# Performance work log

Measured on AMD Instinct MI355X. Metric: run time of the kernel, lower is better.

## Reference

```python
import jax, jax.numpy as jnp
import numpy as np

N_Q = 32   # query window / partition increment
N_K = 128  # key window length
H = 8      # heads


def _ln(x, w=None, b=None, eps=1e-5):
    m = jnp.mean(x, axis=-1, keepdims=True)
    v = jnp.var(x, axis=-1, keepdims=True)
    y = (x - m) * jax.lax.rsqrt(v + eps)
    if w is not None:
        y = y * w
    if b is not None:
        y = y + b
    return y


def setup_inputs() -> dict:
    key = jax.random.key(0)
    ks = jax.random.split(key, 16)
    B, N, C, CP = 1, 2048, 128, 16
    sc = 1.0 / np.sqrt(C)
    inp = {
        "x": jax.random.normal(ks[0], (B, N, C), jnp.float32),
        "s": jax.random.normal(ks[1], (B, N, C), jnp.float32),
        "pair": jax.random.normal(ks[2], (B, N, N, CP), jnp.float32),
        "adaln_s_w": jnp.ones((C,), jnp.float32),
        "adaln_gate_w": jax.random.normal(ks[3], (C, C), jnp.float32) * sc,
        "adaln_gate_b": jnp.zeros((C,), jnp.float32),
        "adaln_skip_w": jax.random.normal(ks[4], (C, C), jnp.float32) * sc,
        "q_w": jax.random.normal(ks[5], (C, C), jnp.float32) * sc,
        "q_b": jnp.zeros((C,), jnp.float32),
        "k_w": jax.random.normal(ks[6], (C, C), jnp.float32) * sc,
        "v_w": jax.random.normal(ks[7], (C, C), jnp.float32) * sc,
        "pair_ln_w": jnp.ones((CP,), jnp.float32),
        "pair_ln_b": jnp.zeros((CP,), jnp.float32),
        "pair_proj_w": jax.random.normal(ks[8], (CP, H), jnp.float32) * 0.25,
        "gate_w": jax.random.normal(ks[9], (C, C), jnp.float32) * sc,
        "attn_proj_w": jax.random.normal(ks[10], (C, C), jnp.float32) * sc,
        "out_w": jax.random.normal(ks[11], (C, C), jnp.float32) * sc,
        "out_b": jnp.full((C,), -2.0, jnp.float32),
    }
    return inp


def reference(x, s, pair, adaln_s_w, adaln_gate_w, adaln_gate_b, adaln_skip_w,
              q_w, q_b, k_w, v_w, pair_ln_w, pair_ln_b, pair_proj_w,
              gate_w, attn_proj_w, out_w, out_b):
    B, N, C = x.shape
    nb = N // N_Q          # number of local blocks
    pad = (N_K - N_Q) // 2  # 48: zero halo on each side
    hd = C // H

    # AdaLN: LN(a) no affine; LN(s) scale-only; gate + skip from s
    a = _ln(x)
    sn = _ln(s, adaln_s_w)
    a = jax.nn.sigmoid(sn @ adaln_gate_w + adaln_gate_b) * a + sn @ adaln_skip_w

    q = a @ q_w + q_b
    k = a @ k_w
    v = a @ v_w

    # local windows: window i covers padded[32i : 32i+128]
    idx = N_Q * jnp.arange(nb)[:, None] + jnp.arange(N_K)[None, :]  # [nb, N_K]

    def window(t):  # [B,N,C] -> [B,nb,N_K,C] with zero-padded edges
        tp = jnp.pad(t, ((0, 0), (pad, pad), (0, 0)))
        return tp[:, idx]

    qb = q.reshape(B, nb, N_Q, H, hd).transpose(0, 3, 1, 2, 4)        # [B,H,nb,NQ,hd]
    kb = window(k).reshape(B, nb, N_K, H, hd).transpose(0, 3, 1, 2, 4)
    vb = window(v).reshape(B, nb, N_K, H, hd).transpose(0, 3, 1, 2, 4)

    # pair bias -> local blocks [B,H,nb,NQ,NK]
    pb = _ln(pair, pair_ln_w, pair_ln_b) @ pair_proj_w                # [B,N,N,H]
    pb = pb.reshape(B, nb, N_Q, N, H)
    pb = jnp.pad(pb, ((0, 0), (0, 0), (0, 0), (pad, pad), (0, 0)))
    pb = jnp.take_along_axis(pb, idx[None, :, None, :, None], axis=3)  # [B,nb,NQ,NK,H]
    bias = pb.transpose(0, 4, 1, 2, 3)

    logits = jnp.einsum('bhnqd,bhnkd->bhnqk', qb, kb) / jnp.sqrt(jnp.float32(hd)) + bias
    attn = jax.nn.softmax(logits, axis=-1)
    o = jnp.einsum('bhnqk,bhnkd->bhnqd', attn, vb)
    o = o.transpose(0, 2, 3, 1, 4).reshape(B, N, C)

    g = jax.nn.sigmoid(o @ gate_w) * o
    out = g @ attn_proj_w
    out = jax.nn.sigmoid(out @ out_w + out_b) * out
    return out
```

## Files before the change

kernel.cpp:

```cpp
#include <hip/hip_runtime.h>
#include <math.h>

#define NTOK 2048
#define CDIM 128
#define HHEADS 8
#define HDIM 16
#define NQW 32
#define NKW 128
#define PADW 48
#define CPD 16
#define BT 8

__device__ __forceinline__ float sigmoid_(float z){ return 1.0f/(1.0f+__expf(-z)); }
__device__ __forceinline__ float rdlane(float v, int l){
    return __int_as_float(__builtin_amdgcn_readlane(__float_as_int(v), l));
}

__global__ __launch_bounds__(512, 4) void k_front(
    const float* __restrict__ x, const float* __restrict__ s,
    const float* __restrict__ s_w,
    const float* __restrict__ gate_w, const float* __restrict__ gate_b,
    const float* __restrict__ skip_w,
    const float* __restrict__ q_w, const float* __restrict__ q_b,
    const float* __restrict__ k_w, const float* __restrict__ v_w,
    const float* __restrict__ pair, const float* __restrict__ pln_w,
    const float* __restrict__ pln_b, const float* __restrict__ pproj,
    float* __restrict__ qo, float* __restrict__ ko, float* __restrict__ vo,
    float* __restrict__ bias)
{
    __shared__ float act_t[CDIM][10];
    __shared__ float sn_t[CDIM][10];
    __shared__ float part[8][2][BT][CDIM];
    const int tid = threadIdx.x;
    const int bid = blockIdx.x;

    if (bid >= NTOK/BT) {
        #pragma unroll
        for (int rep = 0; rep < 2; ++rep) {
            const int idx = (bid - NTOK/BT) * 1024 + rep*512 + tid;
            const int qg = idx >> 7;
            const int j  = idx & 127;
            const int ib = qg >> 5;
            const int qr = qg & 31;
            const int kg = (ib << 5) - PADW + j;
            float outh[HHEADS] = {0,0,0,0,0,0,0,0};
            if (kg >= 0 && kg < NTOK) {
                const float* p = pair + ((size_t)qg * NTOK + kg) * CPD;
                float buf[CPD];
                float sum = 0.f, ssq = 0.f;
                #pragma unroll
                for (int c = 0; c < CPD; c += 4) {
                    const float4 t4 = *(const float4*)(p + c);
                    buf[c+0]=t4.x; buf[c+1]=t4.y; buf[c+2]=t4.z; buf[c+3]=t4.w;
                    sum += t4.x+t4.y+t4.z+t4.w;
                    ssq += t4.x*t4.x+t4.y*t4.y+t4.z*t4.z+t4.w*t4.w;
                }
                const float m  = sum * (1.0f/CPD);
                const float vr = ssq * (1.0f/CPD) - m*m;
                const float rs = rsqrtf(vr + 1e-5f);
                #pragma unroll
                for (int c = 0; c < CPD; ++c) {
                    const float y = (buf[c]-m)*rs*pln_w[c] + pln_b[c];
                    #pragma unroll
                    for (int h = 0; h < HHEADS; ++h)
                        outh[h] = fmaf(y, pproj[c*HHEADS+h], outh[h]);
                }
            }
            float* bb = bias + ((size_t)(ib*HHEADS)*NQW + qr)*NKW + j;
            #pragma unroll
            for (int h = 0; h < HHEADS; ++h)
                bb[(size_t)h*NQW*NKW] = outh[h];
        }
        return;
    }

    const int tok0 = bid * BT;
    const int w = tid >> 6;
    const int L = tid & 63;

    {
        const float2 xv = *(const float2*)(x + (size_t)(tok0+w)*CDIM + 2*L);
        const float2 yv = *(const float2*)(s + (size_t)(tok0+w)*CDIM + 2*L);
        float sx = xv.x+xv.y, sxx = xv.x*xv.x+xv.y*xv.y;
        float sy = yv.x+yv.y, syy = yv.x*yv.x+yv.y*yv.y;
        #pragma unroll
        for (int m = 1; m < 64; m <<= 1) {
            sx  += __shfl_xor(sx,  m, 64);
            sxx += __shfl_xor(sxx, m, 64);
            sy  += __shfl_xor(sy,  m, 64);
            syy += __shfl_xor(syy, m, 64);
        }
        const float inv = 1.0f/128.0f;
        const float mx = sx*inv, vx = sxx*inv - mx*mx;
        const float my = sy*inv, vy = syy*inv - my*my;
        const float rx = rsqrtf(vx+1e-5f), ry = rsqrtf(vy+1e-5f);
        const float2 swv = *(const float2*)(s_w + 2*L);
        act_t[2*L][w]   = (xv.x-mx)*rx;
        act_t[2*L+1][w] = (xv.y-mx)*rx;
        sn_t[2*L][w]    = (yv.x-my)*ry*swv.x;
        sn_t[2*L+1][w]  = (yv.y-my)*ry*swv.y;
    }
    __syncthreads();

    const int i0 = w * 16;
    float snr0 = sn_t[i0 + (L>>3)][L&7];
    float snr1 = sn_t[i0 + 8 + (L>>3)][L&7];

    float ag[8][2] = {{0}}, as_[8][2] = {{0}};
    #pragma unroll
    for (int ii = 0; ii < 16; ++ii) {
        const float2 wg  = *(const float2*)(gate_w + (size_t)(i0+ii)*CDIM + 2*L);
        const float2 wsk = *(const float2*)(skip_w + (size_t)(i0+ii)*CDIM + 2*L);
        #pragma unroll
        for (int t = 0; t < 8; ++t) {
            const int v = ii*8 + t;
            const float a = rdlane((v < 64) ? snr0 : snr1, v & 63);
            ag[t][0]  = fmaf(a, wg.x,  ag[t][0]);
            ag[t][1]  = fmaf(a, wg.y,  ag[t][1]);
            as_[t][0] = fmaf(a, wsk.x, as_[t][0]);
            as_[t][1] = fmaf(a, wsk.y, as_[t][1]);
        }
    }
    #pragma unroll
    for (int t = 0; t < 8; ++t) {
        *(float2*)&part[w][0][t][2*L] = make_float2(ag[t][0],  ag[t][1]);
        *(float2*)&part[w][1][t][2*L] = make_float2(as_[t][0], as_[t][1]);
    }
    __syncthreads();

    const int j  = tid & 127;
    const int tq = tid >> 7;
    {
        float zg[2] = {0,0}, zs[2] = {0,0};
        #pragma unroll
        for (int ww = 0; ww < 8; ++ww) {
            #pragma unroll
            for (int tt = 0; tt < 2; ++tt) {
                zg[tt] += part[ww][0][2*tq+tt][j];
                zs[tt] += part[ww][1][2*tq+tt][j];
            }
        }
        const float gb = gate_b[j];
        const float2 av = *(const float2*)&act_t[j][2*tq];
        const float a2x = sigmoid_(zg[0]+gb)*av.x + zs[0];
        const float a2y = sigmoid_(zg[1]+gb)*av.y + zs[1];
        *(float2*)&sn_t[j][2*tq] = make_float2(a2x, a2y);
    }
    __syncthreads();

    float ar0 = sn_t[i0 + (L>>3)][L&7];
    float ar1 = sn_t[i0 + 8 + (L>>3)][L&7];
    float aq[8][2] = {{0}}, ak[8][2] = {{0}}, avv[8][2] = {{0}};
    #pragma unroll
    for (int ii = 0; ii < 16; ++ii) {
        const float2 wq = *(const float2*)(q_w + (size_t)(i0+ii)*CDIM + 2*L);
        const float2 wk = *(const float2*)(k_w + (size_t)(i0+ii)*CDIM + 2*L);
        const float2 wv = *(const float2*)(v_w + (size_t)(i0+ii)*CDIM + 2*L);
        #pragma unroll
        for (int t = 0; t < 8; ++t) {
            const int v = ii*8 + t;
            const float a = rdlane((v < 64) ? ar0 : ar1, v & 63);
            aq[t][0]  = fmaf(a, wq.x, aq[t][0]);
            aq[t][1]  = fmaf(a, wq.y, aq[t][1]);
            ak[t][0]  = fmaf(a, wk.x, ak[t][0]);
            ak[t][1]  = fmaf(a, wk.y, ak[t][1]);
            avv[t][0] = fmaf(a, wv.x, avv[t][0]);
            avv[t][1] = fmaf(a, wv.y, avv[t][1]);
        }
    }
    #pragma unroll
    for (int t = 0; t < 8; ++t) {
        *(float2*)&part[w][0][t][2*L] = make_float2(aq[t][0], aq[t][1]);
        *(float2*)&part[w][1][t][2*L] = make_float2(ak[t][0], ak[t][1]);
    }
    __syncthreads();
    {
        float zq[2] = {0,0}, zk[2] = {0,0};
        #pragma unroll
        for (int ww = 0; ww < 8; ++ww) {
            #pragma unroll
            for (int tt = 0; tt < 2; ++tt) {
                zq[tt] += part[ww][0][2*tq+tt][j];
                zk[tt] += part[ww][1][2*tq+tt][j];
            }
        }
        const float qbj = q_b[j];
        #pragma unroll
        for (int tt = 0; tt < 2; ++tt) {
            const size_t row = (size_t)(tok0 + 2*tq + tt)*CDIM + j;
            qo[row] = zq[tt] + qbj;
            ko[row] = zk[tt];
        }
    }
    __syncthreads();
    #pragma unroll
    for (int t = 0; t < 8; ++t)
        *(float2*)&part[w][0][t][2*L] = make_float2(avv[t][0], avv[t][1]);
    __syncthreads();
    {
        float zv[2] = {0,0};
        #pragma unroll
        for (int ww = 0; ww < 8; ++ww) {
            #pragma unroll
            for (int tt = 0; tt < 2; ++tt)
                zv[tt] += part[ww][0][2*tq+tt][j];
        }
        #pragma unroll
        for (int tt = 0; tt < 2; ++tt)
            vo[(size_t)(tok0 + 2*tq + tt)*CDIM + j] = zv[tt];
    }
}

__global__ __launch_bounds__(256) void k_attn(
    const float* __restrict__ qi, const float* __restrict__ ki,
    const float* __restrict__ vi, const float* __restrict__ bias,
    float* __restrict__ o)
{
    __shared__ float khs[NKW*20];
    __shared__ float vts[HDIM*132];
    __shared__ float Pms[NQW*132];
    const int ib = blockIdx.x;
    const int h  = blockIdx.y;
    const int t  = threadIdx.x;

    {
        const int jr  = t >> 1;
        const int d08 = (t & 1) * 8;
        const int kg  = ib*NQW - PADW + jr;
        float4 k0 = {0,0,0,0}, k1 = {0,0,0,0};
        float4 v0 = {0,0,0,0}, v1 = {0,0,0,0};
        if (kg >= 0 && kg < NTOK) {
            const float* sk = ki + (size_t)kg*CDIM + h*HDIM + d08;
            const float* sv = vi + (size_t)kg*CDIM + h*HDIM + d08;
            k0 = *(const float4*)sk;  k1 = *(const float4*)(sk+4);
            v0 = *(const float4*)sv;  v1 = *(const float4*)(sv+4);
        }
        *(float4*)&khs[jr*20 + d08]     = k0;
        *(float4*)&khs[jr*20 + d08 + 4] = k1;
        vts[(d08+0)*132 + jr] = v0.x;
        vts[(d08+1)*132 + jr] = v0.y;
        vts[(d08+2)*132 + jr] = v0.z;
        vts[(d08+3)*132 + jr] = v0.w;
        vts[(d08+4)*132 + jr] = v1.x;
        vts[(d08+5)*132 + jr] = v1.y;
        vts[(d08+6)*132 + jr] = v1.z;
        vts[(d08+7)*132 + jr] = v1.w;
    }
    __syncthreads();

    {
        const int rp = t >> 4;
        const int ln = t & 15;
        const int q0 = 2*rp;
        float4 qv[2][4];
        #pragma unroll
        for (int i = 0; i < 2; ++i) {
            const float4* qp = (const float4*)(qi + (size_t)(ib*NQW + q0 + i)*CDIM + h*HDIM);
            #pragma unroll
            for (int dq = 0; dq < 4; ++dq) qv[i][dq] = qp[dq];
        }
        const float* br = bias + ((size_t)(ib*HHEADS + h)*NQW + q0)*NKW;
        float acc[2][8];
        #pragma unroll
        for (int m2 = 0; m2 < 8; ++m2) {
            const int k = ln + 16*m2;
            const float4 c0 = *(const float4*)&khs[k*20];
            const float4 c1 = *(const float4*)&khs[k*20 + 4];
            const float4 c2 = *(const float4*)&khs[k*20 + 8];
            const float4 c3 = *(const float4*)&khs[k*20 + 12];
            #pragma unroll
            for (int i = 0; i < 2; ++i) {
                float sdot = qv[i][0].x*c0.x;
                sdot = fmaf(qv[i][0].y, c0.y, sdot);
                sdot = fmaf(qv[i][0].z, c0.z, sdot);
                sdot = fmaf(qv[i][0].w, c0.w, sdot);
                sdot = fmaf(qv[i][1].x, c1.x, sdot);
                sdot = fmaf(qv[i][1].y, c1.y, sdot);
                sdot = fmaf(qv[i][1].z, c1.z, sdot);
                sdot = fmaf(qv[i][1].w, c1.w, sdot);
                sdot = fmaf(qv[i][2].x, c2.x, sdot);
                sdot = fmaf(qv[i][2].y, c2.y, sdot);
                sdot = fmaf(qv[i][2].z, c2.z, sdot);
                sdot = fmaf(qv[i][2].w, c2.w, sdot);
                sdot = fmaf(qv[i][3].x, c3.x, sdot);
                sdot = fmaf(qv[i][3].y, c3.y, sdot);
                sdot = fmaf(qv[i][3].z, c3.z, sdot);
                sdot = fmaf(qv[i][3].w, c3.w, sdot);
                acc[i][m2] = sdot*0.25f + br[(size_t)i*NKW + k];
            }
        }
        #pragma unroll
        for (int i = 0; i < 2; ++i) {
            float mx = acc[i][0];
            #pragma unroll
            for (int m2 = 1; m2 < 8; ++m2) mx = fmaxf(mx, acc[i][m2]);
            mx = fmaxf(mx, __shfl_xor(mx, 1, 64));
            mx = fmaxf(mx, __shfl_xor(mx, 2, 64));
            mx = fmaxf(mx, __shfl_xor(mx, 4, 64));
            mx = fmaxf(mx, __shfl_xor(mx, 8, 64));
            float sm = 0.f;
            #pragma unroll
            for (int m2 = 0; m2 < 8; ++m2) { acc[i][m2] = __expf(acc[i][m2]-mx); sm += acc[i][m2]; }
            sm += __shfl_xor(sm, 1, 64);
            sm += __shfl_xor(sm, 2, 64);
            sm += __shfl_xor(sm, 4, 64);
            sm += __shfl_xor(sm, 8, 64);
            const float invs = 1.0f / sm;
            #pragma unroll
            for (int m2 = 0; m2 < 8; ++m2)
                Pms[(q0+i)*132 + ln + 16*m2] = acc[i][m2]*invs;
        }
    }
    __syncthreads();

    {
        const int qr = t >> 3, d0 = t & 7;
        const float* pr  = &Pms[qr*132];
        const float* vp0 = &vts[d0*132];
        const float* vp1 = &vts[(d0+8)*132];
        float a0 = 0.f, a1 = 0.f;
        #pragma unroll
        for (int k4 = 0; k4 < 32; ++k4) {
            const float4 pm = *(const float4*)(pr  + 4*k4);
            const float4 u0 = *(const float4*)(vp0 + 4*k4);
            const float4 u1 = *(const float4*)(vp1 + 4*k4);
            a0 = fmaf(pm.x, u0.x, a0); a0 = fmaf(pm.y, u0.y, a0);
            a0 = fmaf(pm.z, u0.z, a0); a0 = fmaf(pm.w, u0.w, a0);
            a1 = fmaf(pm.x, u1.x, a1); a1 = fmaf(pm.y, u1.y, a1);
            a1 = fmaf(pm.z, u1.z, a1); a1 = fmaf(pm.w, u1.w, a1);
        }
        float* dst = o + (size_t)(ib*NQW + qr)*CDIM + h*HDIM;
        dst[d0]   = a0;
        dst[d0+8] = a1;
    }
}

__global__ __launch_bounds__(512) void k_back(
    const float* __restrict__ oin, const float* __restrict__ gate_w,
    const float* __restrict__ proj_w, const float* __restrict__ out_w,
    const float* __restrict__ out_b, float* __restrict__ out)
{
    __shared__ float b0_t[CDIM][10];
    __shared__ float b1_t[CDIM][10];
    __shared__ float part[8][BT][CDIM];
    const int tid = threadIdx.x;
    const int tok0 = blockIdx.x * BT;
    const int w = tid >> 6, L = tid & 63;
    const int j = tid & 127, tq = tid >> 7;

    {
        const float2 ov = *(const float2*)(oin + (size_t)tok0*CDIM + 2*tid);
        const int e = 2*tid, c = e & 127, t = e >> 7;
        b0_t[c][t]   = ov.x;
        b0_t[c+1][t] = ov.y;
    }
    __syncthreads();

    const int i0 = w * 16;

    {
        const float r0 = b0_t[i0 + (L>>3)][L&7];
        const float r1 = b0_t[i0 + 8 + (L>>3)][L&7];
        float acc[8][2] = {{0}};
        #pragma unroll
        for (int ii = 0; ii < 16; ++ii) {
            const float2 wv = *(const float2*)(gate_w + (size_t)(i0+ii)*CDIM + 2*L);
            #pragma unroll
            for (int t = 0; t < 8; ++t) {
                const int v = ii*8 + t;
                const float a = rdlane((v < 64) ? r0 : r1, v & 63);
                acc[t][0] = fmaf(a, wv.x, acc[t][0]);
                acc[t][1] = fmaf(a, wv.y, acc[t][1]);
            }
        }
        #pragma unroll
        for (int t = 0; t < 8; ++t)
            *(float2*)&part[w][t][2*L] = make_float2(acc[t][0], acc[t][1]);
    }
    __syncthreads();
    {
        float z[2] = {0,0};
        #pragma unroll
        for (int ww = 0; ww < 8; ++ww) {
            z[0] += part[ww][2*tq][j];
            z[1] += part[ww][2*tq+1][j];
        }
        const float2 ov = *(const float2*)&b0_t[j][2*tq];
        *(float2*)&b1_t[j][2*tq] = make_float2(sigmoid_(z[0])*ov.x, sigmoid_(z[1])*ov.y);
    }
    __syncthreads();

    {
        const float r0 = b1_t[i0 + (L>>3)][L&7];
        const float r1 = b1_t[i0 + 8 + (L>>3)][L&7];
        float acc[8][2] = {{0}};
        #pragma unroll
        for (int ii = 0; ii < 16; ++ii) {
            const float2 wv = *(const float2*)(proj_w + (size_t)(i0+ii)*CDIM + 2*L);
            #pragma unroll
            for (int t = 0; t < 8; ++t) {
                const int v = ii*8 + t;
                const float a = rdlane((v < 64) ? r0 : r1, v & 63);
                acc[t][0] = fmaf(a, wv.x, acc[t][0]);
                acc[t][1] = fmaf(a, wv.y, acc[t][1]);
            }
        }
        #pragma unroll
        for (int t = 0; t < 8; ++t)
            *(float2*)&part[w][t][2*L] = make_float2(acc[t][0], acc[t][1]);
    }
    __syncthreads();
    float t2v[2];
    {
        float z[2] = {0,0};
        #pragma unroll
        for (int ww = 0; ww < 8; ++ww) {
            z[0] += part[ww][2*tq][j];
            z[1] += part[ww][2*tq+1][j];
        }
        t2v[0] = z[0]; t2v[1] = z[1];
        *(float2*)&b0_t[j][2*tq] = make_float2(z[0], z[1]);
    }
    __syncthreads();

    {
        const float r0 = b0_t[i0 + (L>>3)][L&7];
        const float r1 = b0_t[i0 + 8 + (L>>3)][L&7];
        float acc[8][2] = {{0}};
        #pragma unroll
        for (int ii = 0; ii < 16; ++ii) {
            const float2 wv = *(const float2*)(out_w + (size_t)(i0+ii)*CDIM + 2*L);
            #pragma unroll
            for (int t = 0; t < 8; ++t) {
                const int v = ii*8 + t;
                const float a = rdlane((v < 64) ? r0 : r1, v & 63);
                acc[t][0] = fmaf(a, wv.x, acc[t][0]);
                acc[t][1] = fmaf(a, wv.y, acc[t][1]);
            }
        }
        #pragma unroll
        for (int t = 0; t < 8; ++t)
            *(float2*)&part[w][t][2*L] = make_float2(acc[t][0], acc[t][1]);
    }
    __syncthreads();
    {
        float z[2] = {0,0};
        #pragma unroll
        for (int ww = 0; ww < 8; ++ww) {
            z[0] += part[ww][2*tq][j];
            z[1] += part[ww][2*tq+1][j];
        }
        const float ob = out_b[j];
        out[(size_t)(tok0 + 2*tq)*CDIM + j]     = sigmoid_(z[0]+ob)*t2v[0];
        out[(size_t)(tok0 + 2*tq + 1)*CDIM + j] = sigmoid_(z[1]+ob)*t2v[1];
    }
}

extern "C" void kernel_launch(void* const* d_in, const int* in_sizes, int n_in,
                              void* d_out, int out_size, void* d_ws, size_t ws_size,
                              hipStream_t stream) {
    (void)in_sizes; (void)n_in; (void)out_size; (void)ws_size;
    const float* x           = (const float*)d_in[0];
    const float* s           = (const float*)d_in[1];
    const float* pair        = (const float*)d_in[2];
    const float* adaln_s_w   = (const float*)d_in[3];
    const float* adaln_gate_w= (const float*)d_in[4];
    const float* adaln_gate_b= (const float*)d_in[5];
    const float* adaln_skip_w= (const float*)d_in[6];
    const float* q_w         = (const float*)d_in[7];
    const float* q_b         = (const float*)d_in[8];
    const float* k_w         = (const float*)d_in[9];
    const float* v_w         = (const float*)d_in[10];
    const float* pair_ln_w   = (const float*)d_in[11];
    const float* pair_ln_b   = (const float*)d_in[12];
    const float* pair_proj_w = (const float*)d_in[13];
    const float* gate_w      = (const float*)d_in[14];
    const float* attn_proj_w = (const float*)d_in[15];
    const float* out_w       = (const float*)d_in[16];
    const float* out_b       = (const float*)d_in[17];
    float* out = (float*)d_out;

    float* ws = (float*)d_ws;
    float* q_ws    = ws;
    float* k_ws    = ws + 262144;
    float* v_ws    = ws + 524288;
    float* o_ws    = ws + 786432;
    float* bias_ws = ws + 1048576;

    k_front<<<NTOK/BT + (NTOK*NKW)/1024, 512, 0, stream>>>(
        x, s, adaln_s_w, adaln_gate_w, adaln_gate_b, adaln_skip_w,
        q_w, q_b, k_w, v_w, pair, pair_ln_w, pair_ln_b, pair_proj_w,
        q_ws, k_ws, v_ws, bias_ws);
    k_attn<<<dim3(NTOK/NQW, HHEADS), 256, 0, stream>>>(q_ws, k_ws, v_ws, bias_ws, o_ws);
    k_back<<<NTOK/BT, 512, 0, stream>>>(o_ws, gate_w, attn_proj_w, out_w, out_b, out);
}
```

Measured before the change: 34.42 us.

## Keep softmax probabilities in registers and reduce PV via butterfly shuffles

The attention kernel no longer writes normalized probabilities to shared memory or uses a second barrier and separate PV phase. Each thread multiplies its unnormalized probabilities by V rows held in row-major shared memory and accumulates 16-wide partial outputs. A butterfly shuffle transpose-reduce across the 16 lanes then gives each lane one output dimension, and normalization happens at the end. This removes the P round trip through shared memory and one sync, at the cost of more registers and shuffle instructions.

```diff
diff --git a/kernel.cpp b/kernel.cpp
--- a/kernel.cpp
+++ b/kernel.cpp
@@ -217,8 +217,7 @@
     float* __restrict__ o)
 {
     __shared__ float khs[NKW*20];
-    __shared__ float vts[HDIM*132];
-    __shared__ float Pms[NQW*132];
+    __shared__ float vhs[NKW*20];
     const int ib = blockIdx.x;
     const int h  = blockIdx.y;
     const int t  = threadIdx.x;
@@ -237,102 +236,148 @@
         }
         *(float4*)&khs[jr*20 + d08]     = k0;
         *(float4*)&khs[jr*20 + d08 + 4] = k1;
-        vts[(d08+0)*132 + jr] = v0.x;
-        vts[(d08+1)*132 + jr] = v0.y;
-        vts[(d08+2)*132 + jr] = v0.z;
-        vts[(d08+3)*132 + jr] = v0.w;
-        vts[(d08+4)*132 + jr] = v1.x;
-        vts[(d08+5)*132 + jr] = v1.y;
-        vts[(d08+6)*132 + jr] = v1.z;
-        vts[(d08+7)*132 + jr] = v1.w;
-    }
-    __syncthreads();
-
-    {
-        const int rp = t >> 4;
-        const int ln = t & 15;
-        const int q0 = 2*rp;
-        float4 qv[2][4];
+        *(float4*)&vhs[jr*20 + d08]     = v0;
+        *(float4*)&vhs[jr*20 + d08 + 4] = v1;
+    }
+    __syncthreads();
+
+    const int rp = t >> 4;
+    const int ln = t & 15;
+    const int q0 = 2*rp;
+
+    float4 qv[2][4];
+    #pragma unroll
+    for (int i = 0; i < 2; ++i) {
+        const float4* qp = (const float4*)(qi + (size_t)(ib*NQW + q0 + i)*CDIM + h*HDIM);
+        #pragma unroll
+        for (int dq = 0; dq < 4; ++dq) qv[i][dq] = qp[dq];
+    }
+
+    const float* br = bias + ((size_t)(ib*HHEADS + h)*NQW + q0)*NKW;
+    float p[2][8];
+    #pragma unroll
+    for (int m2 = 0; m2 < 8; ++m2) {
+        const int k = ln + 16*m2;
+        const float4 c0 = *(const float4*)&khs[k*20];
+        const float4 c1 = *(const float4*)&khs[k*20 + 4];
+        const float4 c2 = *(const float4*)&khs[k*20 + 8];
+        const float4 c3 = *(const float4*)&khs[k*20 + 12];
         #pragma unroll
         for (int i = 0; i < 2; ++i) {
-            const float4* qp = (const float4*)(qi + (size_t)(ib*NQW + q0 + i)*CDIM + h*HDIM);
-            #pragma unroll
-            for (int dq = 0; dq < 4; ++dq) qv[i][dq] = qp[dq];
-        }
-        const float* br = bias + ((size_t)(ib*HHEADS + h)*NQW + q0)*NKW;
-        float acc[2][8];
-        #pragma unroll
-        for (int m2 = 0; m2 < 8; ++m2) {
-            const int k = ln + 16*m2;
-            const float4 c0 = *(const float4*)&khs[k*20];
-            const float4 c1 = *(const float4*)&khs[k*20 + 4];
-            const float4 c2 = *(const float4*)&khs[k*20 + 8];
-            const float4 c3 = *(const float4*)&khs[k*20 + 12];
-            #pragma unroll
-            for (int i = 0; i < 2; ++i) {
-                float sdot = qv[i][0].x*c0.x;
-                sdot = fmaf(qv[i][0].y, c0.y, sdot);
-                sdot = fmaf(qv[i][0].z, c0.z, sdot);
-                sdot = fmaf(qv[i][0].w, c0.w, sdot);
-                sdot = fmaf(qv[i][1].x, c1.x, sdot);
-                sdot = fmaf(qv[i][1].y, c1.y, sdot);
-                sdot = fmaf(qv[i][1].z, c1.z, sdot);
-                sdot = fmaf(qv[i][1].w, c1.w, sdot);
-                sdot = fmaf(qv[i][2].x, c2.x, sdot);
-                sdot = fmaf(qv[i][2].y, c2.y, sdot);
-                sdot = fmaf(qv[i][2].z, c2.z, sdot);
-                sdot = fmaf(qv[i][2].w, c2.w, sdot);
-                sdot = fmaf(qv[i][3].x, c3.x, sdot);
-                sdot = fmaf(qv[i][3].y, c3.y, sdot);
-                sdot = fmaf(qv[i][3].z, c3.z, sdot);
-                sdot = fmaf(qv[i][3].w, c3.w, sdot);
-                acc[i][m2] = sdot*0.25f + br[(size_t)i*NKW + k];
-            }
-        }
-        #pragma unroll
-        for (int i = 0; i < 2; ++i) {
-            float mx = acc[i][0];
-            #pragma unroll
-            for (int m2 = 1; m2 < 8; ++m2) mx = fmaxf(mx, acc[i][m2]);
-            mx = fmaxf(mx, __shfl_xor(mx, 1, 64));
-            mx = fmaxf(mx, __shfl_xor(mx, 2, 64));
-            mx = fmaxf(mx, __shfl_xor(mx, 4, 64));
-            mx = fmaxf(mx, __shfl_xor(mx, 8, 64));
-            float sm = 0.f;
-            #pragma unroll
-            for (int m2 = 0; m2 < 8; ++m2) { acc[i][m2] = __expf(acc[i][m2]-mx); sm += acc[i][m2]; }
-            sm += __shfl_xor(sm, 1, 64);
-            sm += __shfl_xor(sm, 2, 64);
-            sm += __shfl_xor(sm, 4, 64);
-            sm += __shfl_xor(sm, 8, 64);
-            const float invs = 1.0f / sm;
-            #pragma unroll
-            for (int m2 = 0; m2 < 8; ++m2)
-                Pms[(q0+i)*132 + ln + 16*m2] = acc[i][m2]*invs;
-        }
-    }
-    __syncthreads();
-
-    {
-        const int qr = t >> 3, d0 = t & 7;
-        const float* pr  = &Pms[qr*132];
-        const float* vp0 = &vts[d0*132];
-        const float* vp1 = &vts[(d0+8)*132];
-        float a0 = 0.f, a1 = 0.f;
-        #pragma unroll
-        for (int k4 = 0; k4 < 32; ++k4) {
-            const float4 pm = *(const float4*)(pr  + 4*k4);
-            const float4 u0 = *(const float4*)(vp0 + 4*k4);
-            const float4 u1 = *(const float4*)(vp1 + 4*k4);
-            a0 = fmaf(pm.x, u0.x, a0); a0 = fmaf(pm.y, u0.y, a0);
-            a0 = fmaf(pm.z, u0.z, a0); a0 = fmaf(pm.w, u0.w, a0);
-            a1 = fmaf(pm.x, u1.x, a1); a1 = fmaf(pm.y, u1.y, a1);
-            a1 = fmaf(pm.z, u1.z, a1); a1 = fmaf(pm.w, u1.w, a1);
-        }
-        float* dst = o + (size_t)(ib*NQW + qr)*CDIM + h*HDIM;
-        dst[d0]   = a0;
-        dst[d0+8] = a1;
-    }
+            float sdot = qv[i][0].x*c0.x;
+            sdot = fmaf(qv[i][0].y, c0.y, sdot);
+            sdot = fmaf(qv[i][0].z, c0.z, sdot);
+            sdot = fmaf(qv[i][0].w, c0.w, sdot);
+            sdot = fmaf(qv[i][1].x, c1.x, sdot);
+            sdot = fmaf(qv[i][1].y, c1.y, sdot);
+            sdot = fmaf(qv[i][1].z, c1.z, sdot);
+            sdot = fmaf(qv[i][1].w, c1.w, sdot);
+            sdot = fmaf(qv[i][2].x, c2.x, sdot);
+            sdot = fmaf(qv[i][2].y, c2.y, sdot);
+            sdot = fmaf(qv[i][2].z, c2.z, sdot);
+            sdot = fmaf(qv[i][2].w, c2.w, sdot);
+            sdot = fmaf(qv[i][3].x, c3.x, sdot);
+            sdot = fmaf(qv[i][3].y, c3.y, sdot);
+            sdot = fmaf(qv[i][3].z, c3.z, sdot);
+            sdot = fmaf(qv[i][3].w, c3.w, sdot);
+            p[i][m2] = sdot*0.25f + br[(size_t)i*NKW + k];
+        }
+    }
+
+    float smv[2];
+    #pragma unroll
+    for (int i = 0; i < 2; ++i) {
+        float mx = p[i][0];
+        #pragma unroll
+        for (int m2 = 1; m2 < 8; ++m2) mx = fmaxf(mx, p[i][m2]);
+        mx = fmaxf(mx, __shfl_xor(mx, 1, 64));
+        mx = fmaxf(mx, __shfl_xor(mx, 2, 64));
+        mx = fmaxf(mx, __shfl_xor(mx, 4, 64));
+        mx = fmaxf(mx, __shfl_xor(mx, 8, 64));
+        float sm = 0.f;
+        #pragma unroll
+        for (int m2 = 0; m2 < 8; ++m2) { p[i][m2] = __expf(p[i][m2]-mx); sm += p[i][m2]; }
+        sm += __shfl_xor(sm, 1, 64);
+        sm += __shfl_xor(sm, 2, 64);
+        sm += __shfl_xor(sm, 4, 64);
+        sm += __shfl_xor(sm, 8, 64);
+        smv[i] = sm;
+    }
+
+    float ov0[16], ov1[16];
+    #pragma unroll
+    for (int d = 0; d < 16; ++d) { ov0[d] = 0.f; ov1[d] = 0.f; }
+    #pragma unroll
+    for (int m2 = 0; m2 < 8; ++m2) {
+        const int k = ln + 16*m2;
+        const float4 a = *(const float4*)&vhs[k*20];
+        const float4 b = *(const float4*)&vhs[k*20 + 4];
+        const float4 c = *(const float4*)&vhs[k*20 + 8];
+        const float4 d4 = *(const float4*)&vhs[k*20 + 12];
+        const float p0 = p[0][m2], p1 = p[1][m2];
+        ov0[0] = fmaf(p0, a.x, ov0[0]);  ov1[0] = fmaf(p1, a.x, ov1[0]);
+        ov0[1] = fmaf(p0, a.y, ov0[1]);  ov1[1] = fmaf(p1, a.y, ov1[1]);
+        ov0[2] = fmaf(p0, a.z, ov0[2]);  ov1[2] = fmaf(p1, a.z, ov1[2]);
+        ov0[3] = fmaf(p0, a.w, ov0[3]);  ov1[3] = fmaf(p1, a.w, ov1[3]);
+        ov0[4] = fmaf(p0, b.x, ov0[4]);  ov1[4] = fmaf(p1, b.x, ov1[4]);
+        ov0[5] = fmaf(p0, b.y, ov0[5]);  ov1[5] = fmaf(p1, b.y, ov1[5]);
+        ov0[6] = fmaf(p0, b.z, ov0[6]);  ov1[6] = fmaf(p1, b.z, ov1[6]);
+        ov0[7] = fmaf(p0, b.w, ov0[7]);  ov1[7] = fmaf(p1, b.w, ov1[7]);
+        ov0[8] = fmaf(p0, c.x, ov0[8]);  ov1[8] = fmaf(p1, c.x, ov1[8]);
+        ov0[9] = fmaf(p0, c.y, ov0[9]);  ov1[9] = fmaf(p1, c.y, ov1[9]);
+        ov0[10]= fmaf(p0, c.z, ov0[10]); ov1[10]= fmaf(p1, c.z, ov1[10]);
+        ov0[11]= fmaf(p0, c.w, ov0[11]); ov1[11]= fmaf(p1, c.w, ov1[11]);
+        ov0[12]= fmaf(p0, d4.x, ov0[12]); ov1[12]= fmaf(p1, d4.x, ov1[12]);
+        ov0[13]= fmaf(p0, d4.y, ov0[13]); ov1[13]= fmaf(p1, d4.y, ov1[13]);
+        ov0[14]= fmaf(p0, d4.z, ov0[14]); ov1[14]= fmaf(p1, d4.z, ov1[14]);
+        ov0[15]= fmaf(p0, d4.w, ov0[15]); ov1[15]= fmaf(p1, d4.w, ov1[15]);
+    }
+
+    float e0, e1;
+    {
+        float r8a[8], r8b[8];
+        #pragma unroll
+        for (int j2 = 0; j2 < 8; ++j2) {
+            const float lo0 = ov0[j2]   + __shfl_xor(ov0[j2],   8, 64);
+            const float hi0 = ov0[j2+8] + __shfl_xor(ov0[j2+8], 8, 64);
+            r8a[j2] = (ln & 8) ? hi0 : lo0;
+            const float lo1 = ov1[j2]   + __shfl_xor(ov1[j2],   8, 64);
+            const float hi1 = ov1[j2+8] + __shfl_xor(ov1[j2+8], 8, 64);
+            r8b[j2] = (ln & 8) ? hi1 : lo1;
+        }
+        float r4a[4], r4b[4];
+        #pragma unroll
+        for (int j2 = 0; j2 < 4; ++j2) {
+            const float lo0 = r8a[j2]   + __shfl_xor(r8a[j2],   4, 64);
+            const float hi0 = r8a[j2+4] + __shfl_xor(r8a[j2+4], 4, 64);
+            r4a[j2] = (ln & 4) ? hi0 : lo0;
+            const float lo1 = r8b[j2]   + __shfl_xor(r8b[j2],   4, 64);
+            const float hi1 = r8b[j2+4] + __shfl_xor(r8b[j2+4], 4, 64);
+            r4b[j2] = (ln & 4) ? hi1 : lo1;
+        }
+        float r2a[2], r2b[2];
+        #pragma unroll
+        for (int j2 = 0; j2 < 2; ++j2) {
+            const float lo0 = r4a[j2]   + __shfl_xor(r4a[j2],   2, 64);
+            const float hi0 = r4a[j2+2] + __shfl_xor(r4a[j2+2], 2, 64);
+            r2a[j2] = (ln & 2) ? hi0 : lo0;
+            const float lo1 = r4b[j2]   + __shfl_xor(r4b[j2],   2, 64);
+            const float hi1 = r4b[j2+2] + __shfl_xor(r4b[j2+2], 2, 64);
+            r2b[j2] = (ln & 2) ? hi1 : lo1;
+        }
+        {
+            const float lo0 = r2a[0] + __shfl_xor(r2a[0], 1, 64);
+            const float hi0 = r2a[1] + __shfl_xor(r2a[1], 1, 64);
+            e0 = (ln & 1) ? hi0 : lo0;
+            const float lo1 = r2b[0] + __shfl_xor(r2b[0], 1, 64);
+            const float hi1 = r2b[1] + __shfl_xor(r2b[1], 1, 64);
+            e1 = (ln & 1) ? hi1 : lo1;
+        }
+    }
+
+    float* dst = o + (size_t)(ib*NQW + q0)*CDIM + h*HDIM + ln;
+    dst[0]    = e0 * (1.0f / smv[0]);
+    dst[CDIM] = e1 * (1.0f / smv[1]);
 }
 
 __global__ __launch_bounds__(512) void k_back(
```

Result: no change. 34.58 us (+0.5%).
